# Kernel optimization log

Measured on AMD Instinct MI355X. Metric: run time of the kernel, lower is better.

The kernel has to match this reference:

```python
import jax, jax.numpy as jnp
import numpy as np
import math

B, S, D, H = 2, 4096, 128, 8

def setup_inputs() -> dict:
    key = jax.random.key(0)
    k1, k2, k3, k4 = jax.random.split(key, 4)
    x = jax.random.normal(k1, (B, S, D), dtype=jnp.float32)
    W_q = jax.random.normal(k2, (H, D, D), dtype=jnp.float32) * 0.02
    W_k = jax.random.normal(k3, (H, D, D), dtype=jnp.float32) * 0.02
    # nn.Linear weight: [out_features, in_features] = [D, D*H]
    W_o = jax.random.normal(k4, (D, D * H), dtype=jnp.float32) * (0.02 / math.sqrt(2 * 12))
    return {"x": x, "W_q": W_q, "W_k": W_k, "W_o": W_o}

def reference(x, W_q, W_k, W_o):
    b, s, d = x.shape
    h = W_q.shape[0]
    # Per-head projections of the same (repeated) input x.
    Q = jnp.einsum('bsd,hde->bhse', x, W_q)          # [B,H,S,D]
    K = jnp.einsum('bsd,hde->bhse', x, W_k)          # [B,H,S,D]
    scores = jnp.einsum('bhse,bhte->bhst', Q, K) / math.sqrt(d)  # [B,H,S,S]
    scores = jnp.clip(scores, -10.0, 10.0)
    causal = jnp.tril(jnp.ones((s, s), dtype=bool))  # [S,S]
    scores = jnp.where(causal[None, None], scores, -jnp.inf)
    attn = jax.nn.softmax(scores, axis=-1)           # dropout p=0 -> identity
    y = jnp.einsum('bhst,btd->bhsd', attn, x)        # V == x per head
    y = jnp.transpose(y, (0, 2, 1, 3)).reshape(b, s, h * d)  # [B,S,H*D]
    out = y @ W_o.T                                  # [B,S,D]
    return out
```

## Files before the change

kernel.cpp:

```cpp
#include <hip/hip_runtime.h>
#include <hip/hip_bf16.h>

typedef unsigned short u16;
typedef unsigned int u32;
typedef __attribute__((ext_vector_type(8))) short bf16x8;
typedef __attribute__((ext_vector_type(4))) float f32x4;
typedef __attribute__((ext_vector_type(16))) float f32x16;
typedef __attribute__((ext_vector_type(2))) unsigned int u32x2;
typedef __attribute__((ext_vector_type(4))) unsigned int u32x4;

#define S_LEN 4096
#define DHEAD 128
#define NHEAD 8
#define NBATCH 2

__device__ __forceinline__ u16 f2b(float f) {
  __hip_bfloat16 h = __float2bfloat16(f);
  return *(u16*)&h;
}

__device__ __forceinline__ f32x4 mfma16(bf16x8 a, bf16x8 b, f32x4 c) {
  return __builtin_amdgcn_mfma_f32_16x16x32_bf16(a, b, c, 0, 0, 0);
}
__device__ __forceinline__ f32x16 mfma32(bf16x8 a, bf16x8 b, f32x16 c) {
  return __builtin_amdgcn_mfma_f32_32x32x16_bf16(a, b, c, 0, 0, 0);
}

__device__ __forceinline__ f32x4 zero4() { f32x4 z = {0.f, 0.f, 0.f, 0.f}; return z; }

__device__ __forceinline__ u32 cvtpk(float lo, float hi) {
  u32 r;
  asm("v_cvt_pk_bf16_f32 %0, %1, %2" : "=v"(r) : "v"(lo), "v"(hi));
  return r;
}
__device__ __forceinline__ u32x2 pswap(u32 a, u32 b) {
  return __builtin_amdgcn_permlane32_swap(a, b, false, false);
}

__device__ __forceinline__ void gll16(const u16* g, u16* l) {
  __builtin_amdgcn_global_load_lds(
      (const __attribute__((address_space(1))) u32*)g,
      (__attribute__((address_space(3))) u32*)l, 16, 0, 0);
}

__global__ void k_conv_x(const float* __restrict__ x, u16* __restrict__ xb,
                         u16* __restrict__ VbF) {
  int idx = blockIdx.x * blockDim.x + threadIdx.x;
  float v = x[idx];
  u16 bv = f2b(v);
  xb[idx] = bv;
  int d = idx & 127;
  int bs = idx >> 7;
  int b = bs >> 12;
  int s = bs & 4095;
  int t64 = s >> 6, kh = (s >> 5) & 1, m2 = (s >> 4) & 1;
  int h5v = (s >> 3) & 1, j = s & 7;
  int db = d >> 5;
  int l = (d & 31) + 32 * h5v;
  int g = kh * 8 + m2 * 4 + db;
  VbF[(((size_t)b * 64 + t64) * 16 + g) * 512 + l * 8 + j] = bv;
}

__global__ void k_conv_w(const float* __restrict__ Wq, const float* __restrict__ Wk,
                         const float* __restrict__ Wo, u16* __restrict__ Wqt,
                         u16* __restrict__ Wkt, u16* __restrict__ WoB) {
  int idx = blockIdx.x * blockDim.x + threadIdx.x;
  int h = idx >> 14;
  int d = (idx >> 7) & 127;
  int e = idx & 127;
  int t = (h << 14) + (e << 7) + d;
  Wqt[t] = f2b(Wq[idx]);
  Wkt[t] = f2b(Wk[idx]);
  WoB[idx] = f2b(Wo[idx]);
}

__global__ __launch_bounds__(256) void k_proj(const u16* __restrict__ xb,
                                              const u16* __restrict__ Wqt,
                                              const u16* __restrict__ Wkt,
                                              u16* __restrict__ Qb, u16* __restrict__ KbF) {
  int wid = threadIdx.x >> 6;
  int lane = threadIdx.x & 63;
  int qt = blockIdx.x * 4 + wid;
  int h = blockIdx.y, z = blockIdx.z;
  int b = z >> 1, w = z & 1;
  int bh = b * NHEAD + h;
  int row16 = lane & 15, kgrp = lane >> 4;
  int sb = qt * 32;
  const u16* xp = xb + ((size_t)b * S_LEN + sb) * DHEAD;
  bf16x8 a[2][4];
#pragma unroll
  for (int r = 0; r < 2; ++r)
#pragma unroll
    for (int kc = 0; kc < 4; ++kc)
      a[r][kc] = *(const bf16x8*)(xp + (r * 16 + row16) * DHEAD + kc * 32 + kgrp * 8);

  const u16* Wt = (w == 0 ? Wqt : Wkt) + (size_t)h * DHEAD * DHEAD;
  f32x4 acc[2][8];
#pragma unroll
  for (int r = 0; r < 2; ++r)
#pragma unroll
    for (int nc = 0; nc < 8; ++nc) acc[r][nc] = zero4();
#pragma unroll
  for (int kc = 0; kc < 4; ++kc)
#pragma unroll
    for (int nc = 0; nc < 8; ++nc) {
      bf16x8 bw = *(const bf16x8*)(Wt + (nc * 16 + row16) * DHEAD + kc * 32 + kgrp * 8);
      acc[0][nc] = mfma16(a[0][kc], bw, acc[0][nc]);
      acc[1][nc] = mfma16(a[1][kc], bw, acc[1][nc]);
    }
  if (w == 0) {
    u16* Out = Qb + ((size_t)bh * S_LEN + sb) * DHEAD;
#pragma unroll
    for (int r = 0; r < 2; ++r)
#pragma unroll
      for (int nc = 0; nc < 8; ++nc)
#pragma unroll
        for (int i = 0; i < 4; ++i)
          Out[(size_t)(r * 16 + kgrp * 4 + i) * DHEAD + nc * 16 + row16] =
              f2b(acc[r][nc][i]);
  } else {
#pragma unroll
    for (int r = 0; r < 2; ++r)
#pragma unroll
      for (int nc = 0; nc < 8; ++nc)
#pragma unroll
        for (int i = 0; i < 4; ++i) {
          int key = sb + r * 16 + kgrp * 4 + i;
          int e = nc * 16 + row16;
          int t64 = key >> 6, kh = (key >> 5) & 1;
          int m = e >> 4;
          int l = (key & 31) + 32 * ((e >> 3) & 1);
          int j = e & 7;
          int f = kh * 8 + m;
          KbF[(((size_t)bh * 64 + t64) * 16 + f) * 512 + l * 8 + j] = f2b(acc[r][nc][i]);
        }
  }
}

__global__ __launch_bounds__(512) void k_attn(const u16* __restrict__ Qb,
                                              const u16* __restrict__ KbF,
                                              const u16* __restrict__ VbF,
                                              u16* __restrict__ Yb) {
  int p = blockIdx.x;
  int xcd = p & 7;
  int j2 = p >> 3;
  int bh = xcd + (j2 >= 16 ? 8 : 0);
  int qpj = j2 & 15;
  int b = bh >> 3, h = bh & 7;

  int tid = threadIdx.x;
  int wid = tid >> 6;
  int lane = tid & 63;
  int qr = wid >> 1;
  int kh = wid & 1;
  int l31 = lane & 31, h5 = lane >> 5;

  __shared__ __align__(16) u16 SMEM[4][8192];
  __shared__ float rsbuf[2][4][32];

  const u16* Kbase = KbF + (size_t)bh * 64 * 16 * 512;
  const u16* Vbase = VbF + (size_t)b * 64 * 16 * 512;

  auto issue = [&](int k0, int buf) {
    const u16* Ks = Kbase + (size_t)(k0 >> 6) * 16 * 512;
#pragma unroll
    for (int fi = 0; fi < 2; ++fi) {
      int f = wid * 2 + fi;
      gll16(Ks + f * 512 + lane * 8, &SMEM[buf][f * 512]);
    }
  };
  auto vload = [&](bf16x8 (&dst)[8], int k0) {
    const u16* Vs = Vbase + ((size_t)(k0 >> 6) * 16 + kh * 8) * 512 + lane * 8;
#pragma unroll
    for (int g = 0; g < 8; ++g) dst[g] = *(const bf16x8*)(Vs + g * 512);
  };

  const float c2 = 0.12754274816295166f;
  const float clip2 = 14.426950408889634f;

  auto runSeg = [&](int qblk) {
    int qb0 = qblk * 128;
    int qw = qb0 + qr * 32;
    int qrow = qw + l31;
    const u16* Qp = Qb + ((size_t)bh * S_LEN + qw) * DHEAD;

    bf16x8 bq[8];
#pragma unroll
    for (int m = 0; m < 8; ++m)
      bq[m] = *(const bf16x8*)(Qp + (size_t)l31 * DHEAD + m * 16 + h5 * 8);

    f32x16 y0, y1, y2, y3;
#pragma unroll
    for (int i = 0; i < 16; ++i) { y0[i] = 0.f; y1[i] = 0.f; y2[i] = 0.f; y3[i] = 0.f; }
    float rs = 0.f;

    bf16x8 vA[8], vB[8];

    auto tilecomp = [&](int buf, int k0, bf16x8 (&vc)[8]) {
      f32x16 sc;
#pragma unroll
      for (int i = 0; i < 16; ++i) sc[i] = 0.f;
      __builtin_amdgcn_s_setprio(1);
#pragma unroll
      for (int m = 0; m < 8; ++m) {
        bf16x8 kf = *(const bf16x8*)&SMEM[buf][((kh * 8 + m) * 512) + lane * 8];
        sc = mfma32(kf, bq[m], sc);
      }
      __builtin_amdgcn_s_setprio(0);

      float pf[16];
      int kb = k0 + kh * 32 + h5 * 4;
      bool nomask = (k0 + kh * 32 + 31) <= qw;
      if (nomask) {
#pragma unroll
        for (int reg = 0; reg < 16; ++reg) {
          float v = __builtin_amdgcn_fmed3f(sc[reg] * c2, -clip2, clip2);
          float pc = __builtin_amdgcn_exp2f(v);
          rs += pc;
          pf[reg] = pc;
        }
      } else {
#pragma unroll
        for (int reg = 0; reg < 16; ++reg) {
          int key = kb + (reg & 3) + 8 * (reg >> 2);
          float v = __builtin_amdgcn_fmed3f(sc[reg] * c2, -clip2, clip2);
          float pc = __builtin_amdgcn_exp2f(v);
          pc = (key > qrow) ? 0.0f : pc;
          rs += pc;
          pf[reg] = pc;
        }
      }
      u32 cv0 = cvtpk(pf[0], pf[1]), cv1 = cvtpk(pf[2], pf[3]);
      u32 cv2 = cvtpk(pf[4], pf[5]), cv3 = cvtpk(pf[6], pf[7]);
      u32 cv4 = cvtpk(pf[8], pf[9]), cv5 = cvtpk(pf[10], pf[11]);
      u32 cv6 = cvtpk(pf[12], pf[13]), cv7 = cvtpk(pf[14], pf[15]);
      u32x2 s0 = pswap(cv0, cv2);
      u32x2 s1 = pswap(cv1, cv3);
      u32x2 s2 = pswap(cv4, cv6);
      u32x2 s3 = pswap(cv5, cv7);
      u32x4 pa0u = {s0.x, s1.x, s0.y, s1.y};
      u32x4 pa1u = {s2.x, s3.x, s2.y, s3.y};
      bf16x8 pa0 = __builtin_bit_cast(bf16x8, pa0u);
      bf16x8 pa1 = __builtin_bit_cast(bf16x8, pa1u);
      __builtin_amdgcn_s_setprio(1);
      y0 = mfma32(pa0, vc[0], y0);
      y0 = mfma32(pa1, vc[4], y0);
      y1 = mfma32(pa0, vc[1], y1);
      y1 = mfma32(pa1, vc[5], y1);
      y2 = mfma32(pa0, vc[2], y2);
      y2 = mfma32(pa1, vc[6], y2);
      y3 = mfma32(pa0, vc[3], y3);
      y3 = mfma32(pa1, vc[7], y3);
      __builtin_amdgcn_s_setprio(0);
    };

    int NT = 2 * qblk + 2;
    issue(0, 0);
    issue(64, 1);
    vload(vA, 0);
    __syncthreads();
    for (int t = 0; t < NT; t += 2) {
      int k0 = t * 64;
      vload(vB, k0 + 64);
      if (t + 2 < NT) issue(k0 + 128, (t + 2) & 3);
      if (t + 3 < NT) issue(k0 + 192, (t + 3) & 3);
      __builtin_amdgcn_sched_barrier(0);
      tilecomp(t & 3, k0, vA);
      if (t + 2 < NT) vload(vA, k0 + 128);
      __builtin_amdgcn_sched_barrier(0);
      tilecomp((t + 1) & 3, k0 + 64, vB);
      asm volatile("s_waitcnt vmcnt(8)" ::: "memory");
      __builtin_amdgcn_s_barrier();
      __builtin_amdgcn_sched_barrier(0);
    }

    rs += __shfl_xor(rs, 32, 64);

    float* scr = (float*)&SMEM[0][0] + qr * 4096;
    if (kh == 1) {
#pragma unroll
      for (int db = 0; db < 4; ++db) {
        const f32x16& yv = (db == 0) ? y0 : (db == 1) ? y1 : (db == 2) ? y2 : y3;
#pragma unroll
        for (int r4 = 0; r4 < 4; ++r4) {
          f32x4 ch = {yv[r4 * 4 + 0], yv[r4 * 4 + 1], yv[r4 * 4 + 2], yv[r4 * 4 + 3]};
          *(f32x4*)&scr[((db * 4 + r4) * 64 + lane) * 4] = ch;
        }
      }
      if (lane < 32) rsbuf[1][qr][lane] = rs;
    }
    __syncthreads();
    if (kh == 0) {
      float rs2 = rs + rsbuf[1][qr][l31];
      float inv = 1.0f / rs2;
      if (lane < 32) rsbuf[0][qr][lane] = inv;
#pragma unroll
      for (int db = 0; db < 4; ++db) {
        f32x16& yv = (db == 0) ? y0 : (db == 1) ? y1 : (db == 2) ? y2 : y3;
#pragma unroll
        for (int r4 = 0; r4 < 4; ++r4) {
          f32x4 ch = *(const f32x4*)&scr[((db * 4 + r4) * 64 + lane) * 4];
#pragma unroll
          for (int k = 0; k < 4; ++k) yv[r4 * 4 + k] += ch[k];
        }
      }
      u16* Yp = Yb + ((size_t)b * S_LEN + qw) * (NHEAD * DHEAD) + h * DHEAD;
#pragma unroll
      for (int db = 0; db < 4; ++db) {
        const f32x16& yv = (db == 0) ? y0 : (db == 1) ? y1 : (db == 2) ? y2 : y3;
#pragma unroll
        for (int reg = 0; reg < 16; ++reg) {
          int qp2 = (reg & 3) + 8 * (reg >> 2) + 4 * h5;
          float rv = rsbuf[0][qr][qp2];
          Yp[(size_t)qp2 * (NHEAD * DHEAD) + db * 32 + l31] = f2b(yv[reg] * rv);
        }
      }
    }
    __syncthreads();
  };

  runSeg(31 - qpj);
  runSeg(qpj);
}

__global__ __launch_bounds__(256) void k_oproj(const u16* __restrict__ Yb,
                                               const u16* __restrict__ WoB,
                                               float* __restrict__ out) {
  int wid = threadIdx.x >> 6;
  int lane = threadIdx.x & 63;
  int mb = (blockIdx.x * 4 + wid) * 32 + blockIdx.y * 16;
  int nb = blockIdx.z * 64;
  int row16 = lane & 15, kgrp = lane >> 4;
  f32x4 acc[4];
#pragma unroll
  for (int nc = 0; nc < 4; ++nc) acc[nc] = zero4();
#pragma unroll 4
  for (int kc = 0; kc < 32; ++kc) {
    bf16x8 a0 = *(const bf16x8*)(Yb + (size_t)(mb + row16) * 1024 + kc * 32 + kgrp * 8);
#pragma unroll
    for (int nc = 0; nc < 4; ++nc) {
      bf16x8 bw =
          *(const bf16x8*)(WoB + (size_t)(nb + nc * 16 + row16) * 1024 + kc * 32 + kgrp * 8);
      acc[nc] = mfma16(a0, bw, acc[nc]);
    }
  }
#pragma unroll
  for (int nc = 0; nc < 4; ++nc)
#pragma unroll
    for (int i = 0; i < 4; ++i)
      out[(size_t)(mb + kgrp * 4 + i) * DHEAD + nb + nc * 16 + row16] = acc[nc][i];
}

extern "C" void kernel_launch(void* const* d_in, const int* in_sizes, int n_in,
                              void* d_out, int out_size, void* d_ws, size_t ws_size,
                              hipStream_t stream) {
  const float* x = (const float*)d_in[0];
  const float* Wq = (const float*)d_in[1];
  const float* Wk = (const float*)d_in[2];
  const float* Wo = (const float*)d_in[3];
  float* out = (float*)d_out;

  char* ws = (char*)d_ws;
  size_t off = 0;
  auto alloc = [&](size_t bytes) -> void* {
    void* p = ws + off;
    off += (bytes + 255) & ~(size_t)255;
    return p;
  };
  const size_t nx = (size_t)NBATCH * S_LEN * DHEAD;
  const size_t nqk = (size_t)NBATCH * NHEAD * S_LEN * DHEAD;
  u16* xb = (u16*)alloc(nx * 2);
  u16* VbF = (u16*)alloc(nx * 2);
  u16* Wqt = (u16*)alloc((size_t)NHEAD * DHEAD * DHEAD * 2);
  u16* Wkt = (u16*)alloc((size_t)NHEAD * DHEAD * DHEAD * 2);
  u16* WoB = (u16*)alloc((size_t)DHEAD * NHEAD * DHEAD * 2);
  u16* Qb = (u16*)alloc(nqk * 2);
  u16* KbF = (u16*)alloc(nqk * 2);
  u16* Yb = (u16*)alloc(nqk * 2);
  (void)ws_size;

  k_conv_x<<<dim3(nx / 256), dim3(256), 0, stream>>>(x, xb, VbF);
  k_conv_w<<<dim3(131072 / 256), dim3(256), 0, stream>>>(Wq, Wk, Wo, Wqt, Wkt, WoB);
  k_proj<<<dim3(S_LEN / 32 / 4, NHEAD, 2 * NBATCH), dim3(256), 0, stream>>>(xb, Wqt, Wkt, Qb, KbF);
  k_attn<<<dim3(256), dim3(512), 0, stream>>>(Qb, KbF, VbF, Yb);
  k_oproj<<<dim3((NBATCH * S_LEN) / 32 / 4, 2, 2), dim3(256), 0, stream>>>(Yb, WoB, out);
}
```

Measured before the change: 144.3 us.

## Emit Q/K in MFMA fragment layout via 32x32 MFMA projection, drop xb buffer

The projection kernel now reads fp32 x directly and converts it to bf16 in registers, removing the separate bf16 copy of x. It uses 32x32 MFMA with the weight as the A operand, so the output fragments can be packed with permlane swaps and written as coalesced 16-byte stores in a fragment-ordered layout. Both Q and K use this layout, and the attention kernel now loads Q fragments contiguously. The V conversion kernel is rewritten so each thread gathers 8 strided fp32 values and writes one vector store, replacing the earlier scattered 2-byte writes. In exchange, each projection wave re-reads fp32 x, and the V gather reads x with a strided pattern.

```diff
diff --git a/kernel.cpp b/kernel.cpp
--- a/kernel.cpp
+++ b/kernel.cpp
@@ -37,28 +37,39 @@
   return __builtin_amdgcn_permlane32_swap(a, b, false, false);
 }
 
+__device__ __forceinline__ void packA(const float* pf, bf16x8& pa0, bf16x8& pa1) {
+  u32 cv0 = cvtpk(pf[0], pf[1]), cv1 = cvtpk(pf[2], pf[3]);
+  u32 cv2 = cvtpk(pf[4], pf[5]), cv3 = cvtpk(pf[6], pf[7]);
+  u32 cv4 = cvtpk(pf[8], pf[9]), cv5 = cvtpk(pf[10], pf[11]);
+  u32 cv6 = cvtpk(pf[12], pf[13]), cv7 = cvtpk(pf[14], pf[15]);
+  u32x2 s0 = pswap(cv0, cv2), s1 = pswap(cv1, cv3);
+  u32x2 s2 = pswap(cv4, cv6), s3 = pswap(cv5, cv7);
+  u32x4 a0 = {s0.x, s1.x, s0.y, s1.y};
+  u32x4 a1 = {s2.x, s3.x, s2.y, s3.y};
+  pa0 = __builtin_bit_cast(bf16x8, a0);
+  pa1 = __builtin_bit_cast(bf16x8, a1);
+}
+
 __device__ __forceinline__ void gll16(const u16* g, u16* l) {
   __builtin_amdgcn_global_load_lds(
       (const __attribute__((address_space(1))) u32*)g,
       (__attribute__((address_space(3))) u32*)l, 16, 0, 0);
 }
 
-__global__ void k_conv_x(const float* __restrict__ x, u16* __restrict__ xb,
-                         u16* __restrict__ VbF) {
+__global__ void k_conv_x(const float* __restrict__ x, u16* __restrict__ VbF) {
   int idx = blockIdx.x * blockDim.x + threadIdx.x;
-  float v = x[idx];
-  u16 bv = f2b(v);
-  xb[idx] = bv;
-  int d = idx & 127;
-  int bs = idx >> 7;
-  int b = bs >> 12;
-  int s = bs & 4095;
-  int t64 = s >> 6, kh = (s >> 5) & 1, m2 = (s >> 4) & 1;
-  int h5v = (s >> 3) & 1, j = s & 7;
-  int db = d >> 5;
-  int l = (d & 31) + 32 * h5v;
-  int g = kh * 8 + m2 * 4 + db;
-  VbF[(((size_t)b * 64 + t64) * 16 + g) * 512 + l * 8 + j] = bv;
+  int b = idx >> 16;
+  int t64 = (idx >> 10) & 63;
+  int g = (idx >> 6) & 15;
+  int l = idx & 63;
+  int kh = g >> 3, m2 = (g >> 2) & 1, db = g & 3;
+  int keyb = t64 * 64 + kh * 32 + m2 * 16 + (l >> 5) * 8;
+  int d = db * 32 + (l & 31);
+  const float* xp = x + ((size_t)b * S_LEN + keyb) * DHEAD + d;
+  u16 o[8];
+#pragma unroll
+  for (int j = 0; j < 8; ++j) o[j] = f2b(xp[(size_t)j * DHEAD]);
+  *(bf16x8*)(VbF + (size_t)idx * 8) = *(const bf16x8*)o;
 }
 
 __global__ void k_conv_w(const float* __restrict__ Wq, const float* __restrict__ Wk,
@@ -74,70 +85,57 @@
   WoB[idx] = f2b(Wo[idx]);
 }
 
-__global__ __launch_bounds__(256) void k_proj(const u16* __restrict__ xb,
+__global__ __launch_bounds__(256) void k_proj(const float* __restrict__ x,
                                               const u16* __restrict__ Wqt,
                                               const u16* __restrict__ Wkt,
-                                              u16* __restrict__ Qb, u16* __restrict__ KbF) {
+                                              u16* __restrict__ QbF, u16* __restrict__ KbF) {
   int wid = threadIdx.x >> 6;
   int lane = threadIdx.x & 63;
   int qt = blockIdx.x * 4 + wid;
   int h = blockIdx.y, z = blockIdx.z;
   int b = z >> 1, w = z & 1;
   int bh = b * NHEAD + h;
-  int row16 = lane & 15, kgrp = lane >> 4;
+  int l31 = lane & 31, h5 = lane >> 5;
   int sb = qt * 32;
-  const u16* xp = xb + ((size_t)b * S_LEN + sb) * DHEAD;
-  bf16x8 a[2][4];
-#pragma unroll
-  for (int r = 0; r < 2; ++r)
-#pragma unroll
-    for (int kc = 0; kc < 4; ++kc)
-      a[r][kc] = *(const bf16x8*)(xp + (r * 16 + row16) * DHEAD + kc * 32 + kgrp * 8);
+
+  const float* xp = x + ((size_t)b * S_LEN + sb + l31) * DHEAD;
+  bf16x8 bx[8];
+#pragma unroll
+  for (int dk = 0; dk < 8; ++dk) {
+    f32x4 lo = *(const f32x4*)(xp + dk * 16 + h5 * 8);
+    f32x4 hi = *(const f32x4*)(xp + dk * 16 + h5 * 8 + 4);
+    u32x4 pk = {cvtpk(lo[0], lo[1]), cvtpk(lo[2], lo[3]),
+                cvtpk(hi[0], hi[1]), cvtpk(hi[2], hi[3])};
+    bx[dk] = __builtin_bit_cast(bf16x8, pk);
+  }
 
   const u16* Wt = (w == 0 ? Wqt : Wkt) + (size_t)h * DHEAD * DHEAD;
-  f32x4 acc[2][8];
-#pragma unroll
-  for (int r = 0; r < 2; ++r)
-#pragma unroll
-    for (int nc = 0; nc < 8; ++nc) acc[r][nc] = zero4();
-#pragma unroll
-  for (int kc = 0; kc < 4; ++kc)
-#pragma unroll
-    for (int nc = 0; nc < 8; ++nc) {
-      bf16x8 bw = *(const bf16x8*)(Wt + (nc * 16 + row16) * DHEAD + kc * 32 + kgrp * 8);
-      acc[0][nc] = mfma16(a[0][kc], bw, acc[0][nc]);
-      acc[1][nc] = mfma16(a[1][kc], bw, acc[1][nc]);
-    }
-  if (w == 0) {
-    u16* Out = Qb + ((size_t)bh * S_LEN + sb) * DHEAD;
-#pragma unroll
-    for (int r = 0; r < 2; ++r)
-#pragma unroll
-      for (int nc = 0; nc < 8; ++nc)
-#pragma unroll
-        for (int i = 0; i < 4; ++i)
-          Out[(size_t)(r * 16 + kgrp * 4 + i) * DHEAD + nc * 16 + row16] =
-              f2b(acc[r][nc][i]);
-  } else {
-#pragma unroll
-    for (int r = 0; r < 2; ++r)
-#pragma unroll
-      for (int nc = 0; nc < 8; ++nc)
-#pragma unroll
-        for (int i = 0; i < 4; ++i) {
-          int key = sb + r * 16 + kgrp * 4 + i;
-          int e = nc * 16 + row16;
-          int t64 = key >> 6, kh = (key >> 5) & 1;
-          int m = e >> 4;
-          int l = (key & 31) + 32 * ((e >> 3) & 1);
-          int j = e & 7;
-          int f = kh * 8 + m;
-          KbF[(((size_t)bh * 64 + t64) * 16 + f) * 512 + l * 8 + j] = f2b(acc[r][nc][i]);
-        }
+  u16* Out = (w == 0 ? QbF : KbF);
+  size_t obase = (w == 0)
+                     ? ((size_t)(bh * 128 + qt) * 8) * 512
+                     : (((size_t)bh * 64 + (qt >> 1)) * 16 + (qt & 1) * 8) * 512;
+
+#pragma unroll
+  for (int eb = 0; eb < 4; ++eb) {
+    f32x16 sc;
+#pragma unroll
+    for (int i = 0; i < 16; ++i) sc[i] = 0.f;
+#pragma unroll
+    for (int dk = 0; dk < 8; ++dk) {
+      bf16x8 aw = *(const bf16x8*)(Wt + (size_t)(eb * 32 + l31) * DHEAD + dk * 16 + h5 * 8);
+      sc = mfma32(aw, bx[dk], sc);
+    }
+    float pf[16];
+#pragma unroll
+    for (int i = 0; i < 16; ++i) pf[i] = sc[i];
+    bf16x8 pa0, pa1;
+    packA(pf, pa0, pa1);
+    *(bf16x8*)(Out + obase + (size_t)(eb * 2 + 0) * 512 + lane * 8) = pa0;
+    *(bf16x8*)(Out + obase + (size_t)(eb * 2 + 1) * 512 + lane * 8) = pa1;
   }
 }
 
-__global__ __launch_bounds__(512) void k_attn(const u16* __restrict__ Qb,
+__global__ __launch_bounds__(512) void k_attn(const u16* __restrict__ QbF,
                                               const u16* __restrict__ KbF,
                                               const u16* __restrict__ VbF,
                                               u16* __restrict__ Yb) {
@@ -182,12 +180,12 @@
     int qb0 = qblk * 128;
     int qw = qb0 + qr * 32;
     int qrow = qw + l31;
-    const u16* Qp = Qb + ((size_t)bh * S_LEN + qw) * DHEAD;
+    const u16* Qp = QbF + ((size_t)(bh * 128 + (qw >> 5)) * 8) * 512;
 
     bf16x8 bq[8];
 #pragma unroll
     for (int m = 0; m < 8; ++m)
-      bq[m] = *(const bf16x8*)(Qp + (size_t)l31 * DHEAD + m * 16 + h5 * 8);
+      bq[m] = *(const bf16x8*)(Qp + (size_t)m * 512 + lane * 8);
 
     f32x16 y0, y1, y2, y3;
 #pragma unroll
@@ -230,18 +228,8 @@
           pf[reg] = pc;
         }
       }
-      u32 cv0 = cvtpk(pf[0], pf[1]), cv1 = cvtpk(pf[2], pf[3]);
-      u32 cv2 = cvtpk(pf[4], pf[5]), cv3 = cvtpk(pf[6], pf[7]);
-      u32 cv4 = cvtpk(pf[8], pf[9]), cv5 = cvtpk(pf[10], pf[11]);
-      u32 cv6 = cvtpk(pf[12], pf[13]), cv7 = cvtpk(pf[14], pf[15]);
-      u32x2 s0 = pswap(cv0, cv2);
-      u32x2 s1 = pswap(cv1, cv3);
-      u32x2 s2 = pswap(cv4, cv6);
-      u32x2 s3 = pswap(cv5, cv7);
-      u32x4 pa0u = {s0.x, s1.x, s0.y, s1.y};
-      u32x4 pa1u = {s2.x, s3.x, s2.y, s3.y};
-      bf16x8 pa0 = __builtin_bit_cast(bf16x8, pa0u);
-      bf16x8 pa1 = __builtin_bit_cast(bf16x8, pa1u);
+      bf16x8 pa0, pa1;
+      packA(pf, pa0, pa1);
       __builtin_amdgcn_s_setprio(1);
       y0 = mfma32(pa0, vc[0], y0);
       y0 = mfma32(pa1, vc[4], y0);
@@ -369,19 +357,18 @@
   };
   const size_t nx = (size_t)NBATCH * S_LEN * DHEAD;
   const size_t nqk = (size_t)NBATCH * NHEAD * S_LEN * DHEAD;
-  u16* xb = (u16*)alloc(nx * 2);
   u16* VbF = (u16*)alloc(nx * 2);
   u16* Wqt = (u16*)alloc((size_t)NHEAD * DHEAD * DHEAD * 2);
   u16* Wkt = (u16*)alloc((size_t)NHEAD * DHEAD * DHEAD * 2);
   u16* WoB = (u16*)alloc((size_t)DHEAD * NHEAD * DHEAD * 2);
-  u16* Qb = (u16*)alloc(nqk * 2);
+  u16* QbF = (u16*)alloc(nqk * 2);
   u16* KbF = (u16*)alloc(nqk * 2);
   u16* Yb = (u16*)alloc(nqk * 2);
   (void)ws_size;
 
-  k_conv_x<<<dim3(nx / 256), dim3(256), 0, stream>>>(x, xb, VbF);
+  k_conv_x<<<dim3(512), dim3(256), 0, stream>>>(x, VbF);
   k_conv_w<<<dim3(131072 / 256), dim3(256), 0, stream>>>(Wq, Wk, Wo, Wqt, Wkt, WoB);
-  k_proj<<<dim3(S_LEN / 32 / 4, NHEAD, 2 * NBATCH), dim3(256), 0, stream>>>(xb, Wqt, Wkt, Qb, KbF);
-  k_attn<<<dim3(256), dim3(512), 0, stream>>>(Qb, KbF, VbF, Yb);
+  k_proj<<<dim3(S_LEN / 32 / 4, NHEAD, 2 * NBATCH), dim3(256), 0, stream>>>(x, Wqt, Wkt, QbF, KbF);
+  k_attn<<<dim3(256), dim3(512), 0, stream>>>(QbF, KbF, VbF, Yb);
   k_oproj<<<dim3((NBATCH * S_LEN) / 32 / 4, 2, 2), dim3(256), 0, stream>>>(Yb, WoB, out);
 }
```

Measured after the change: 142.0 us. No clear change (-1.6%).
